# Performance work log

Measured on AMD Instinct MI355X. Metric: run time of the kernel, lower is better.

Reference implementation:

```python
import jax, jax.numpy as jnp
import numpy as np

B, T, C, H = 4, 2048, 2048, 16
HD = C // H  # head_size = 128
EPS = 1e-5


def layernorm(x, g, b):
    mu = jnp.mean(x, axis=-1, keepdims=True)
    var = jnp.var(x, axis=-1, keepdims=True)
    return (x - mu) * jax.lax.rsqrt(var + EPS) * g + b


def setup_inputs() -> dict:
    key = jax.random.key(0)
    ks = jax.random.split(key, 12)
    s_attn = 1.0 / np.sqrt(C)
    s_ffn1 = 1.0 / np.sqrt(C)
    s_ffn2 = 1.0 / np.sqrt(4 * C)
    return {
        "x": jax.random.normal(ks[0], (B, T, C), jnp.float32),
        "Wq": jax.random.normal(ks[1], (H, C, HD), jnp.float32) * s_attn,
        "Wk": jax.random.normal(ks[2], (H, C, HD), jnp.float32) * s_attn,
        "Wv": jax.random.normal(ks[3], (H, C, HD), jnp.float32) * s_attn,
        "Wp": jax.random.normal(ks[4], (C, C), jnp.float32) * s_attn,
        "bp": jnp.zeros((C,), jnp.float32),
        "W1": jax.random.normal(ks[5], (C, 4 * C), jnp.float32) * s_ffn1,
        "b1": jnp.zeros((4 * C,), jnp.float32),
        "W2": jax.random.normal(ks[6], (4 * C, C), jnp.float32) * s_ffn2,
        "b2": jnp.zeros((C,), jnp.float32),
        "g1": jnp.ones((C,), jnp.float32),
        "beta1": jnp.zeros((C,), jnp.float32),
        "g2": jnp.ones((C,), jnp.float32),
        "beta2": jnp.zeros((C,), jnp.float32),
    }


def reference(x, Wq, Wk, Wv, Wp, bp, W1, b1, W2, b2, g1, beta1, g2, beta2):
    # --- attention sublayer (pre-LN, causal) ---
    h = layernorm(x, g1, beta1)
    q = jnp.einsum("btc,hcd->bhtd", h, Wq)
    k = jnp.einsum("bsc,hcd->bhsd", h, Wk)
    v = jnp.einsum("bsc,hcd->bhsd", h, Wv)
    scores = jnp.einsum("bhtd,bhsd->bhts", q, k) / jnp.sqrt(jnp.asarray(HD, x.dtype))
    causal = jnp.tril(jnp.ones((T, T), bool))
    scores = jnp.where(causal, scores, jnp.asarray(-jnp.inf, x.dtype))
    w = jax.nn.softmax(scores, axis=-1)  # dropout = identity (eval mode)
    o = jnp.einsum("bhts,bhsd->bhtd", w, v)
    o = o.transpose(0, 2, 1, 3).reshape(B, T, C)  # concat heads
    x = x + o @ Wp + bp
    # --- feed-forward sublayer ---
    h2 = layernorm(x, g2, beta2)
    f = jax.nn.gelu(h2 @ W1 + b1, approximate=False)
    x = x + f @ W2 + b2
    return x
```

## Files before the change

kernel.cpp:

```cpp
#include <hip/hip_runtime.h>
#include <math.h>

#define B_ 4
#define T_ 2048
#define C_ 2048
#define H_ 16
#define HD_ 128

typedef __attribute__((ext_vector_type(8))) short short8;
typedef __attribute__((ext_vector_type(4))) float f32x4;
typedef unsigned short u16;
typedef unsigned int u32;

__device__ __forceinline__ u16 f2bf(float f) {
  union { float f; unsigned u; } v; v.f = f;
  unsigned r = v.u + 0x7FFFu + ((v.u >> 16) & 1u);
  return (u16)(r >> 16);
}

__device__ __forceinline__ u16 f2bf_trunc(float f) {
  union { float f; unsigned u; } v; v.f = f;
  return (u16)(v.u >> 16);
}

__device__ __forceinline__ void gld16(const void* g, void* l) {
  __builtin_amdgcn_global_load_lds(
      (__attribute__((address_space(1))) void*)(void*)g,
      (__attribute__((address_space(3))) void*)l, 16, 0, 0);
}

__global__ __launch_bounds__(256) void tconv(const float* __restrict__ in,
                                             u16* __restrict__ out,
                                             int K, int N,
                                             long inBS, long outBS) {
  __shared__ float tile[32][33];
  const float* inb = in + (long)blockIdx.z * inBS;
  u16* outb = out + (long)blockIdx.z * outBS;
  int k0 = blockIdx.x << 5, n0 = blockIdx.y << 5;
  int t = threadIdx.x;
  {
    int kk = t >> 3, nn = (t & 7) << 2;
    float4 v = *(const float4*)(inb + (long)(k0 + kk) * N + n0 + nn);
    tile[kk][nn + 0] = v.x; tile[kk][nn + 1] = v.y;
    tile[kk][nn + 2] = v.z; tile[kk][nn + 3] = v.w;
  }
  __syncthreads();
  {
    int nn = t >> 3, kk = (t & 7) << 2;
    ushort4 o;
    o.x = f2bf(tile[kk + 0][nn]); o.y = f2bf(tile[kk + 1][nn]);
    o.z = f2bf(tile[kk + 2][nn]); o.w = f2bf(tile[kk + 3][nn]);
    *(ushort4*)(outb + (long)(n0 + nn) * K + k0 + kk) = o;
  }
}

__global__ __launch_bounds__(256) void ln_rows(const float* __restrict__ x,
                                               const float* __restrict__ gam,
                                               const float* __restrict__ bet,
                                               u16* __restrict__ out) {
  int row = blockIdx.x;
  const float* xr = x + (size_t)row * C_;
  int t = threadIdx.x;
  float4 v0 = *(const float4*)(xr + t * 8);
  float4 v1 = *(const float4*)(xr + t * 8 + 4);
  float s = v0.x + v0.y + v0.z + v0.w + v1.x + v1.y + v1.z + v1.w;
  float ss = v0.x * v0.x + v0.y * v0.y + v0.z * v0.z + v0.w * v0.w +
             v1.x * v1.x + v1.y * v1.y + v1.z * v1.z + v1.w * v1.w;
  for (int d = 32; d > 0; d >>= 1) {
    s += __shfl_down(s, d);
    ss += __shfl_down(ss, d);
  }
  __shared__ float red[8];
  int wv = t >> 6;
  if ((t & 63) == 0) { red[wv] = s; red[4 + wv] = ss; }
  __syncthreads();
  s = red[0] + red[1] + red[2] + red[3];
  ss = red[4] + red[5] + red[6] + red[7];
  float mu = s * (1.0f / C_);
  float var = ss * (1.0f / C_) - mu * mu;
  float rs = rsqrtf(var + 1e-5f);
  int c = t * 8;
  float vv[8] = {v0.x, v0.y, v0.z, v0.w, v1.x, v1.y, v1.z, v1.w};
  ushort4 o0, o1;
  o0.x = f2bf((vv[0] - mu) * rs * gam[c + 0] + bet[c + 0]);
  o0.y = f2bf((vv[1] - mu) * rs * gam[c + 1] + bet[c + 1]);
  o0.z = f2bf((vv[2] - mu) * rs * gam[c + 2] + bet[c + 2]);
  o0.w = f2bf((vv[3] - mu) * rs * gam[c + 3] + bet[c + 3]);
  o1.x = f2bf((vv[4] - mu) * rs * gam[c + 4] + bet[c + 4]);
  o1.y = f2bf((vv[5] - mu) * rs * gam[c + 5] + bet[c + 5]);
  o1.z = f2bf((vv[6] - mu) * rs * gam[c + 6] + bet[c + 6]);
  o1.w = f2bf((vv[7] - mu) * rs * gam[c + 7] + bet[c + 7]);
  *(ushort4*)(out + (size_t)row * C_ + c) = o0;
  *(ushort4*)(out + (size_t)row * C_ + c + 4) = o1;
}

template <int EPI>
__global__ __launch_bounds__(512, 2) void gemm256(
    const u16* __restrict__ A, const u16* __restrict__ BT,
    int M, int N, int K, int lda, int ldb,
    u16* __restrict__ oq, u16* __restrict__ ok, u16* __restrict__ ovt,
    float* __restrict__ of32, const float* __restrict__ resid,
    const float* __restrict__ bias, u16* __restrict__ obf, int addBias) {
  extern __shared__ char smem[];
  int nbx = N >> 8;
  int nwg = gridDim.x;
  int flat = blockIdx.x;
  int sw = (flat & 7) * (nwg >> 3) + (flat >> 3);
  int bx = sw % nbx, by = sw / nbx;
  int m0 = by << 8, n0 = bx << 8;
  int tid = threadIdx.x;
  int lane = tid & 63, wave = tid >> 6;
  int wm = wave >> 2, wn = wave & 3;
  int l15 = lane & 15, l16 = lane >> 4;
  int nt = K >> 6;

  f32x4 acc[8][4] = {};
  short8 af[8], bf[4];

  auto stage = [&](int b, int r, int k0) {
    int isB = (r >> 1) & 1;
    int ks = r >> 2;
    int row = (r & 1) * 128 + (tid >> 2);
    int swz = (row & 3) ^ ((row >> 2) & 3);
    int gslot = (tid & 3) ^ swz;
    char* dst = smem + isB * 65536 + b * 32768 + ks * 16384 + (r & 1) * 8192 +
                tid * 16;
    const u16* src = (isB ? (BT + (long)(n0 + row) * ldb)
                          : (A + (long)(m0 + row) * lda)) +
                     k0 + ks * 32 + gslot * 8;
    gld16(src, dst);
  };
  auto ldA = [&](int b, int ks, int mf) {
    int row = wm * 128 + mf * 16 + l15;
    int swz = (row & 3) ^ ((row >> 2) & 3);
    return *(const short8*)(smem + b * 32768 + ks * 16384 + row * 64 +
                            ((l16 ^ swz) << 4));
  };
  auto ldB = [&](int b, int ks, int nf) {
    int row = wn * 64 + nf * 16 + l15;
    int swz = (row & 3) ^ ((row >> 2) & 3);
    return *(const short8*)(smem + 65536 + b * 32768 + ks * 16384 + row * 64 +
                            ((l16 ^ swz) << 4));
  };

#pragma unroll
  for (int r = 0; r < 8; ++r) stage(0, r, 0);
  asm volatile("s_waitcnt vmcnt(4)" ::: "memory");
  __builtin_amdgcn_s_barrier();

  for (int t = 0; t < nt; ++t) {
    int cur = t & 1, nxt = cur ^ 1;
    bool more = (t + 1) < nt;
    int k1 = (t + 1) << 6;
    if (more) {
#pragma unroll
      for (int r = 0; r < 8; ++r) stage(nxt, r, k1);
    }
#pragma unroll
    for (int mf = 0; mf < 8; ++mf) af[mf] = ldA(cur, 0, mf);
#pragma unroll
    for (int nf = 0; nf < 4; ++nf) bf[nf] = ldB(cur, 0, nf);
    __builtin_amdgcn_s_setprio(1);
#pragma unroll
    for (int mf = 0; mf < 8; ++mf)
#pragma unroll
      for (int nf = 0; nf < 4; ++nf)
        acc[mf][nf] = __builtin_amdgcn_mfma_f32_16x16x32_bf16(
            af[mf], bf[nf], acc[mf][nf], 0, 0, 0);
    __builtin_amdgcn_s_setprio(0);
    if (more)
      asm volatile("s_waitcnt vmcnt(8)" ::: "memory");
    else
      asm volatile("s_waitcnt vmcnt(0)" ::: "memory");
    __builtin_amdgcn_s_barrier();
#pragma unroll
    for (int mf = 0; mf < 8; ++mf) af[mf] = ldA(cur, 1, mf);
#pragma unroll
    for (int nf = 0; nf < 4; ++nf) bf[nf] = ldB(cur, 1, nf);
    __builtin_amdgcn_s_setprio(1);
#pragma unroll
    for (int mf = 0; mf < 8; ++mf)
#pragma unroll
      for (int nf = 0; nf < 4; ++nf)
        acc[mf][nf] = __builtin_amdgcn_mfma_f32_16x16x32_bf16(
            af[mf], bf[nf], acc[mf][nf], 0, 0, 0);
    __builtin_amdgcn_s_setprio(0);
    if (more) {
      asm volatile("s_waitcnt vmcnt(4)" ::: "memory");
      __builtin_amdgcn_s_barrier();
    }
  }

#pragma unroll
  for (int mf = 0; mf < 8; ++mf) {
#pragma unroll
    for (int nf = 0; nf < 4; ++nf) {
      int rowf = m0 + wm * 128 + mf * 16 + l16 * 4;
      int col = n0 + wn * 64 + nf * 16 + l15;
      if constexpr (EPI == 0) {
        int seg = col >> 11, cn = col & 2047;
        int hh = cn >> 7, dd = cn & 127;
        int bb = rowf >> 11, t0 = rowf & 2047;
        if (seg == 2) {
          ushort4 o;
          o.x = f2bf(acc[mf][nf][0]); o.y = f2bf(acc[mf][nf][1]);
          o.z = f2bf(acc[mf][nf][2]); o.w = f2bf(acc[mf][nf][3]);
          *(ushort4*)(ovt + ((long)(bb * H_ + hh) * HD_ + dd) * T_ + t0) = o;
        } else if (seg == 0) {
          const float qs = 0.08838834764831845f * 1.4426950408889634f;
#pragma unroll
          for (int r = 0; r < 4; ++r)
            oq[((long)(bb * H_ + hh) * T_ + t0 + r) * HD_ + dd] =
                f2bf(acc[mf][nf][r] * qs);
        } else {
#pragma unroll
          for (int r = 0; r < 4; ++r)
            ok[((long)(bb * H_ + hh) * T_ + t0 + r) * HD_ + dd] =
                f2bf(acc[mf][nf][r]);
        }
      } else if constexpr (EPI == 1) {
#pragma unroll
        for (int r = 0; r < 4; ++r) {
          long idx = (long)(rowf + r) * N + col;
          of32[idx] = resid[idx] + bias[col] + acc[mf][nf][r];
        }
      } else if constexpr (EPI == 2) {
#pragma unroll
        for (int r = 0; r < 4; ++r) {
          float v = acc[mf][nf][r] + bias[col];
          float g = 0.5f * v * (1.0f + erff(v * 0.70710678118654752f));
          obf[(long)(rowf + r) * N + col] = f2bf(g);
        }
      } else {
#pragma unroll
        for (int r = 0; r < 4; ++r) {
          long idx = (long)(rowf + r) * N + col;
          float v = acc[mf][nf][r];
          if (addBias) v += bias[col];
          of32[idx] += v;
        }
      }
    }
  }
}

__global__ __launch_bounds__(256) void attn_fwd(const u16* __restrict__ q,
                                                const u16* __restrict__ k,
                                                const u16* __restrict__ vt,
                                                u16* __restrict__ o) {
  extern __shared__ char asmem[];
  int bid = blockIdx.x;
  int bh = bid & 63;
  int qb = 31 - (bid >> 6);
  int q0 = qb << 6;
  int tid = threadIdx.x, lane = tid & 63, wave = tid >> 6;
  int l15 = lane & 15, l16 = lane >> 4;
  int wq0 = q0 + wave * 16;
  const u16* kbase = k + (long)bh * T_ * HD_;
  const u16* vbase = vt + (long)bh * HD_ * T_;
  char* Psw = asmem + 32768 + wave * 1024;

  short8 qf[4];
#pragma unroll
  for (int kk = 0; kk < 4; ++kk)
    qf[kk] = *(const short8*)(q + ((long)bh * T_ + wq0 + l15) * HD_ +
                              kk * 32 + l16 * 8);

  short8 vone;
#pragma unroll
  for (int j = 0; j < 8; ++j) vone[j] = (short)0x3F80;

  f32x4 accO[8] = {};
  float m_r[4], l_r[4];
#pragma unroll
  for (int r = 0; r < 4; ++r) { m_r[r] = -INFINITY; l_r[r] = 0.f; }

  int nt = 2 * qb + 2;

  auto stage = [&](int b, int t) {
    int s0 = t << 5;
    char* Kd = asmem + b * 8192;
    char* Vd = asmem + 16384 + b * 8192;
#pragma unroll
    for (int r = 0; r < 2; ++r) {
      int off = r * 4096 + tid * 16;
      int krow = off >> 8;
      int kslot = (tid & 15) ^ (krow & 7);
      gld16(kbase + (long)(s0 + krow) * HD_ + kslot * 8, Kd + off);
      int dd = off >> 6;
      int vslot = (tid & 3) ^ (dd & 3);
      gld16(vbase + (long)dd * T_ + s0 + vslot * 8, Vd + off);
    }
  };

  stage(0, 0);
  asm volatile("s_waitcnt vmcnt(0)" ::: "memory");
  __syncthreads();

  for (int t = 0; t < nt; ++t) {
    int s0 = t << 5;
    int cur = t & 1;
    bool more = (t + 1 < nt);
    if (more) stage(cur ^ 1, t + 1);

    if (s0 <= wq0 + 15) {
      const char* Kc = asmem + cur * 8192;
      const char* Vc = asmem + 16384 + cur * 8192;
      bool needmask = (s0 + 31 > wq0);
      f32x4 S[2];
#pragma unroll
      for (int sb = 0; sb < 2; ++sb) {
        f32x4 s = {};
#pragma unroll
        for (int kk = 0; kk < 4; ++kk) {
          int srow = sb * 16 + l15;
          int kb = srow * 256 + (((kk * 4 + l16) ^ (srow & 7)) << 4);
          short8 kf = *(const short8*)(Kc + kb);
          s = __builtin_amdgcn_mfma_f32_16x16x32_bf16(qf[kk], kf, s, 0, 0, 0);
        }
        S[sb] = s;
      }
      float mxl[4];
      bool growL = false;
#pragma unroll
      for (int r = 0; r < 4; ++r) {
        int tt = wq0 + 4 * l16 + r;
        float mx = -INFINITY;
#pragma unroll
        for (int sb = 0; sb < 2; ++sb) {
          float v = S[sb][r];
          if (needmask && (s0 + sb * 16 + l15 > tt)) v = -INFINITY;
          S[sb][r] = v;
          mx = fmaxf(mx, v);
        }
        mxl[r] = mx;
        growL = growL || (mx > m_r[r] + 8.0f);
      }
      bool anyg = __any(growL);
      float al[4];
      if (anyg) {
#pragma unroll
        for (int r = 0; r < 4; ++r) {
          float mx = mxl[r];
          mx = fmaxf(mx, __shfl_xor(mx, 1));
          mx = fmaxf(mx, __shfl_xor(mx, 2));
          mx = fmaxf(mx, __shfl_xor(mx, 4));
          mx = fmaxf(mx, __shfl_xor(mx, 8));
          float mo = m_r[r];
          float mn = fmaxf(mo, mx);
          al[r] = exp2f(mo - mn);
          m_r[r] = mn;
        }
      } else {
#pragma unroll
        for (int r = 0; r < 4; ++r) al[r] = 1.0f;
      }
#pragma unroll
      for (int r = 0; r < 4; ++r) {
        float mn = m_r[r];
        int prow = 4 * l16 + r;
#pragma unroll
        for (int sb = 0; sb < 2; ++sb) {
          float p = exp2f(S[sb][r] - mn);
          int col = sb * 16 + l15;
          int slot = col >> 3;
          int pb = prow * 64 + ((slot ^ l16) << 4) + (col & 7) * 2;
          *(u16*)(Psw + pb) = f2bf_trunc(p);
        }
      }
      if (anyg) {
#pragma unroll
        for (int db = 0; db < 8; ++db)
#pragma unroll
          for (int r = 0; r < 4; ++r) accO[db][r] *= al[r];
      }
      int pslot = l16 ^ ((l15 >> 2) & 3);
      short8 pf = *(const short8*)(Psw + l15 * 64 + (pslot << 4));
      f32x4 zz = {};
      f32x4 sacc = __builtin_amdgcn_mfma_f32_16x16x32_bf16(pf, vone, zz, 0, 0, 0);
#pragma unroll
      for (int r = 0; r < 4; ++r) l_r[r] = l_r[r] * al[r] + sacc[r];
#pragma unroll
      for (int db = 0; db < 8; ++db) {
        int vrow = db * 16 + l15;
        int vb = vrow * 64 + ((l16 ^ (vrow & 3)) << 4);
        short8 vf = *(const short8*)(Vc + vb);
        accO[db] = __builtin_amdgcn_mfma_f32_16x16x32_bf16(pf, vf,
                                                           accO[db], 0, 0, 0);
      }
    }
    if (more) asm volatile("s_waitcnt vmcnt(0)" ::: "memory");
    __syncthreads();
  }

  int bb = bh >> 4, hh = bh & 15;
  float inv[4];
#pragma unroll
  for (int r = 0; r < 4; ++r) inv[r] = 1.0f / l_r[r];
#pragma unroll
  for (int db = 0; db < 8; ++db)
#pragma unroll
    for (int r = 0; r < 4; ++r) {
      int tt = wq0 + 4 * l16 + r;
      o[((long)bb * T_ + tt) * C_ + hh * HD_ + db * 16 + l15] =
          f2bf(accO[db][r] * inv[r]);
    }
}

extern "C" void kernel_launch(void* const* d_in, const int* in_sizes, int n_in,
                              void* d_out, int out_size, void* d_ws, size_t ws_size,
                              hipStream_t stream) {
  (void)in_sizes; (void)n_in; (void)out_size; (void)ws_size;
  const float* x   = (const float*)d_in[0];
  const float* Wq  = (const float*)d_in[1];
  const float* Wk  = (const float*)d_in[2];
  const float* Wv  = (const float*)d_in[3];
  const float* Wp  = (const float*)d_in[4];
  const float* bp  = (const float*)d_in[5];
  const float* W1  = (const float*)d_in[6];
  const float* b1  = (const float*)d_in[7];
  const float* W2  = (const float*)d_in[8];
  const float* b2  = (const float*)d_in[9];
  const float* g1  = (const float*)d_in[10];
  const float* be1 = (const float*)d_in[11];
  const float* g2  = (const float*)d_in[12];
  const float* be2 = (const float*)d_in[13];
  float* out = (float*)d_out;

  (void)hipFuncSetAttribute((const void*)gemm256<0>,
                            hipFuncAttributeMaxDynamicSharedMemorySize, 131072);
  (void)hipFuncSetAttribute((const void*)gemm256<1>,
                            hipFuncAttributeMaxDynamicSharedMemorySize, 131072);
  (void)hipFuncSetAttribute((const void*)gemm256<2>,
                            hipFuncAttributeMaxDynamicSharedMemorySize, 131072);
  (void)hipFuncSetAttribute((const void*)gemm256<3>,
                            hipFuncAttributeMaxDynamicSharedMemorySize, 131072);
  (void)hipFuncSetAttribute((const void*)attn_fwd,
                            hipFuncAttributeMaxDynamicSharedMemorySize, 36864);

  char* ws = (char*)d_ws;
  size_t off = 0;
  auto alloc = [&](size_t n) {
    void* p = ws + off;
    off += (n + 255) & ~(size_t)255;
    return p;
  };
  u16* wqkvT = (u16*)alloc((size_t)6144 * 2048 * 2);
  u16* wpT   = (u16*)alloc((size_t)2048 * 2048 * 2);
  u16* w1T   = (u16*)alloc((size_t)8192 * 2048 * 2);
  u16* w2T   = (u16*)alloc((size_t)2048 * 8192 * 2);
  u16* hb    = (u16*)alloc((size_t)8192 * 2048 * 2);
  u16* qbuf  = (u16*)alloc((size_t)8192 * 2048 * 2);
  u16* kbuf  = (u16*)alloc((size_t)8192 * 2048 * 2);
  u16* vtbuf = (u16*)alloc((size_t)8192 * 2048 * 2);
  u16* ob = hb;
  u16* fb = qbuf;

  tconv<<<dim3(64, 4, 16), 256, 0, stream>>>(Wq, wqkvT, 2048, 128,
                                             (long)2048 * 128, (long)128 * 2048);
  tconv<<<dim3(64, 4, 16), 256, 0, stream>>>(Wk, wqkvT + (size_t)2048 * 2048, 2048, 128,
                                             (long)2048 * 128, (long)128 * 2048);
  tconv<<<dim3(64, 4, 16), 256, 0, stream>>>(Wv, wqkvT + (size_t)4096 * 2048, 2048, 128,
                                             (long)2048 * 128, (long)128 * 2048);
  tconv<<<dim3(64, 64, 1), 256, 0, stream>>>(Wp, wpT, 2048, 2048, 0, 0);
  tconv<<<dim3(64, 256, 1), 256, 0, stream>>>(W1, w1T, 2048, 8192, 0, 0);
  tconv<<<dim3(256, 64, 1), 256, 0, stream>>>(W2, w2T, 8192, 2048, 0, 0);

  ln_rows<<<8192, 256, 0, stream>>>(x, g1, be1, hb);
  gemm256<0><<<768, 512, 131072, stream>>>(hb, wqkvT, 8192, 6144, 2048, 2048, 2048,
                                           qbuf, kbuf, vtbuf, nullptr, nullptr,
                                           nullptr, nullptr, 0);
  attn_fwd<<<2048, 256, 36864, stream>>>(qbuf, kbuf, vtbuf, ob);
  gemm256<1><<<256, 512, 131072, stream>>>(ob, wpT, 8192, 2048, 2048, 2048, 2048,
                                           nullptr, nullptr, nullptr, out, x, bp,
                                           nullptr, 0);

  ln_rows<<<8192, 256, 0, stream>>>(out, g2, be2, hb);
  for (int c = 0; c < 2; ++c) {
    gemm256<2><<<512, 512, 131072, stream>>>(hb, w1T + (size_t)c * 4096 * 2048,
                                             8192, 4096, 2048, 2048, 2048,
                                             nullptr, nullptr, nullptr, nullptr,
                                             nullptr, b1 + c * 4096, fb, 0);
    gemm256<3><<<256, 512, 131072, stream>>>(fb, w2T + (size_t)c * 4096,
                                             8192, 2048, 4096, 4096, 8192,
                                             nullptr, nullptr, nullptr, out,
                                             nullptr, b2, nullptr, c == 0 ? 1 : 0);
  }
}
```

Baseline: 1.252 ms.

## Switch GEMM to triple-buffered K=32 stages with one barrier per step

```diff
diff --git a/kernel.cpp b/kernel.cpp
--- a/kernel.cpp
+++ b/kernel.cpp
@@ -95,7 +95,7 @@
 }
 
 template <int EPI>
-__global__ __launch_bounds__(512, 2) void gemm256(
+__global__ __launch_bounds__(512, 1) void gemm256(
     const u16* __restrict__ A, const u16* __restrict__ BT,
     int M, int N, int K, int lda, int ldb,
     u16* __restrict__ oq, u16* __restrict__ ok, u16* __restrict__ ovt,
@@ -112,81 +112,75 @@
   int lane = tid & 63, wave = tid >> 6;
   int wm = wave >> 2, wn = wave & 3;
   int l15 = lane & 15, l16 = lane >> 4;
-  int nt = K >> 6;
+  int nt = K >> 5;
 
   f32x4 acc[8][4] = {};
-  short8 af[8], bf[4];
+  short8 af[4], bf[4], af2[4];
 
   auto stage = [&](int b, int r, int k0) {
-    int isB = (r >> 1) & 1;
-    int ks = r >> 2;
-    int row = (r & 1) * 128 + (tid >> 2);
-    int swz = (row & 3) ^ ((row >> 2) & 3);
-    int gslot = (tid & 3) ^ swz;
-    char* dst = smem + isB * 65536 + b * 32768 + ks * 16384 + (r & 1) * 8192 +
-                tid * 16;
+    int isB = r >> 1, rr = r & 1;
+    int row = rr * 128 + 2 * (tid >> 3) + ((tid >> 2) & 1);
+    int kslot = (tid & 3) ^ ((tid >> 3) & 3);
+    char* dst = smem + b * 32768 + isB * 16384 + rr * 8192 + tid * 16;
     const u16* src = (isB ? (BT + (long)(n0 + row) * ldb)
                           : (A + (long)(m0 + row) * lda)) +
-                     k0 + ks * 32 + gslot * 8;
+                     k0 + kslot * 8;
     gld16(src, dst);
   };
-  auto ldA = [&](int b, int ks, int mf) {
+  auto ldA = [&](int b, int mf) {
     int row = wm * 128 + mf * 16 + l15;
-    int swz = (row & 3) ^ ((row >> 2) & 3);
-    return *(const short8*)(smem + b * 32768 + ks * 16384 + row * 64 +
-                            ((l16 ^ swz) << 4));
+    int slot = l16 ^ ((row >> 1) & 3);
+    return *(const short8*)(smem + b * 32768 + row * 64 + (slot << 4));
   };
-  auto ldB = [&](int b, int ks, int nf) {
+  auto ldB = [&](int b, int nf) {
     int row = wn * 64 + nf * 16 + l15;
-    int swz = (row & 3) ^ ((row >> 2) & 3);
-    return *(const short8*)(smem + 65536 + b * 32768 + ks * 16384 + row * 64 +
-                            ((l16 ^ swz) << 4));
+    int slot = l16 ^ ((row >> 1) & 3);
+    return *(const short8*)(smem + b * 32768 + 16384 + row * 64 + (slot << 4));
   };
 
 #pragma unroll
-  for (int r = 0; r < 8; ++r) stage(0, r, 0);
+  for (int r = 0; r < 4; ++r) stage(0, r, 0);
+#pragma unroll
+  for (int r = 0; r < 4; ++r) stage(1, r, 32);
   asm volatile("s_waitcnt vmcnt(4)" ::: "memory");
   __builtin_amdgcn_s_barrier();
 
   for (int t = 0; t < nt; ++t) {
-    int cur = t & 1, nxt = cur ^ 1;
-    bool more = (t + 1) < nt;
-    int k1 = (t + 1) << 6;
-    if (more) {
-#pragma unroll
-      for (int r = 0; r < 8; ++r) stage(nxt, r, k1);
-    }
-#pragma unroll
-    for (int mf = 0; mf < 8; ++mf) af[mf] = ldA(cur, 0, mf);
-#pragma unroll
-    for (int nf = 0; nf < 4; ++nf) bf[nf] = ldB(cur, 0, nf);
+    int bi = t % 3;
+    bool s2 = (t + 2) < nt;
+    if (s2) {
+      int b2 = (t + 2) % 3;
+      int k2 = (t + 2) << 5;
+#pragma unroll
+      for (int r = 0; r < 4; ++r) stage(b2, r, k2);
+    }
+#pragma unroll
+    for (int mf = 0; mf < 4; ++mf) af[mf] = ldA(bi, mf);
+#pragma unroll
+    for (int nf = 0; nf < 4; ++nf) bf[nf] = ldB(bi, nf);
+#pragma unroll
+    for (int mf = 0; mf < 4; ++mf) af2[mf] = ldA(bi, 4 + mf);
     __builtin_amdgcn_s_setprio(1);
 #pragma unroll
-    for (int mf = 0; mf < 8; ++mf)
+    for (int mf = 0; mf < 4; ++mf)
 #pragma unroll
       for (int nf = 0; nf < 4; ++nf)
         acc[mf][nf] = __builtin_amdgcn_mfma_f32_16x16x32_bf16(
             af[mf], bf[nf], acc[mf][nf], 0, 0, 0);
     __builtin_amdgcn_s_setprio(0);
-    if (more)
-      asm volatile("s_waitcnt vmcnt(8)" ::: "memory");
-    else
-      asm volatile("s_waitcnt vmcnt(0)" ::: "memory");
-    __builtin_amdgcn_s_barrier();
-#pragma unroll
-    for (int mf = 0; mf < 8; ++mf) af[mf] = ldA(cur, 1, mf);
-#pragma unroll
-    for (int nf = 0; nf < 4; ++nf) bf[nf] = ldB(cur, 1, nf);
     __builtin_amdgcn_s_setprio(1);
 #pragma unroll
-    for (int mf = 0; mf < 8; ++mf)
+    for (int mf = 0; mf < 4; ++mf)
 #pragma unroll
       for (int nf = 0; nf < 4; ++nf)
-        acc[mf][nf] = __builtin_amdgcn_mfma_f32_16x16x32_bf16(
-            af[mf], bf[nf], acc[mf][nf], 0, 0, 0);
+        acc[4 + mf][nf] = __builtin_amdgcn_mfma_f32_16x16x32_bf16(
+            af2[mf], bf[nf], acc[4 + mf][nf], 0, 0, 0);
     __builtin_amdgcn_s_setprio(0);
-    if (more) {
-      asm volatile("s_waitcnt vmcnt(4)" ::: "memory");
+    if ((t + 1) < nt) {
+      if (s2)
+        asm volatile("s_waitcnt vmcnt(4)" ::: "memory");
+      else
+        asm volatile("s_waitcnt vmcnt(0)" ::: "memory");
       __builtin_amdgcn_s_barrier();
     }
   }
@@ -428,13 +422,13 @@
   float* out = (float*)d_out;
 
   (void)hipFuncSetAttribute((const void*)gemm256<0>,
-                            hipFuncAttributeMaxDynamicSharedMemorySize, 131072);
+                            hipFuncAttributeMaxDynamicSharedMemorySize, 98304);
   (void)hipFuncSetAttribute((const void*)gemm256<1>,
-                            hipFuncAttributeMaxDynamicSharedMemorySize, 131072);
+                            hipFuncAttributeMaxDynamicSharedMemorySize, 98304);
   (void)hipFuncSetAttribute((const void*)gemm256<2>,
-                            hipFuncAttributeMaxDynamicSharedMemorySize, 131072);
+                            hipFuncAttributeMaxDynamicSharedMemorySize, 98304);
   (void)hipFuncSetAttribute((const void*)gemm256<3>,
-                            hipFuncAttributeMaxDynamicSharedMemorySize, 131072);
+                            hipFuncAttributeMaxDynamicSharedMemorySize, 98304);
   (void)hipFuncSetAttribute((const void*)attn_fwd,
                             hipFuncAttributeMaxDynamicSharedMemorySize, 36864);
 
@@ -467,23 +461,23 @@
   tconv<<<dim3(256, 64, 1), 256, 0, stream>>>(W2, w2T, 8192, 2048, 0, 0);
 
   ln_rows<<<8192, 256, 0, stream>>>(x, g1, be1, hb);
-  gemm256<0><<<768, 512, 131072, stream>>>(hb, wqkvT, 8192, 6144, 2048, 2048, 2048,
-                                           qbuf, kbuf, vtbuf, nullptr, nullptr,
-                                           nullptr, nullptr, 0);
+  gemm256<0><<<768, 512, 98304, stream>>>(hb, wqkvT, 8192, 6144, 2048, 2048, 2048,
+                                          qbuf, kbuf, vtbuf, nullptr, nullptr,
+                                          nullptr, nullptr, 0);
   attn_fwd<<<2048, 256, 36864, stream>>>(qbuf, kbuf, vtbuf, ob);
-  gemm256<1><<<256, 512, 131072, stream>>>(ob, wpT, 8192, 2048, 2048, 2048, 2048,
-                                           nullptr, nullptr, nullptr, out, x, bp,
-                                           nullptr, 0);
+  gemm256<1><<<256, 512, 98304, stream>>>(ob, wpT, 8192, 2048, 2048, 2048, 2048,
+                                          nullptr, nullptr, nullptr, out, x, bp,
+                                          nullptr, 0);
 
   ln_rows<<<8192, 256, 0, stream>>>(out, g2, be2, hb);
   for (int c = 0; c < 2; ++c) {
-    gemm256<2><<<512, 512, 131072, stream>>>(hb, w1T + (size_t)c * 4096 * 2048,
-                                             8192, 4096, 2048, 2048, 2048,
-                                             nullptr, nullptr, nullptr, nullptr,
-                                             nullptr, b1 + c * 4096, fb, 0);
-    gemm256<3><<<256, 512, 131072, stream>>>(fb, w2T + (size_t)c * 4096,
-                                             8192, 2048, 4096, 4096, 8192,
-                                             nullptr, nullptr, nullptr, out,
-                                             nullptr, b2, nullptr, c == 0 ? 1 : 0);
-  }
-}
+    gemm256<2><<<512, 512, 98304, stream>>>(hb, w1T + (size_t)c * 4096 * 2048,
+                                            8192, 4096, 2048, 2048, 2048,
+                                            nullptr, nullptr, nullptr, nullptr,
+                                            nullptr, b1 + c * 4096, fb, 0);
+    gemm256<3><<<256, 512, 98304, stream>>>(fb, w2T + (size_t)c * 4096,
+                                            8192, 2048, 4096, 4096, 8192,
+                                            nullptr, nullptr, nullptr, out,
+                                            nullptr, b2, nullptr, c == 0 ? 1 : 0);
+  }
+}
```

New measurement: 1.151 ms. 8.1% less time.
